# Kernel optimization log

Measured on AMD Instinct MI355X. Metric: run time of the kernel, lower is better.

Reference implementation:

```python
import jax, jax.numpy as jnp
import numpy as np

ROUTING_ITERS = 3

def squash(t, axis=-1):
    norm = jnp.linalg.norm(t, axis=axis, keepdims=True)
    scale = norm ** 2 / (1 + norm ** 2)
    return scale * t / (norm + 1e-08)

def setup_inputs() -> dict:
    key = jax.random.key(0)
    k1, k2 = jax.random.split(key)
    B, R, C, Din, Dout = 64, 4608, 32, 16, 16
    x = jax.random.normal(k1, (B, R, Din), dtype=jnp.float32)
    route_weights = jax.random.normal(k2, (R, C, Din, Dout), dtype=jnp.float32)
    return {"x": x, "route_weights": route_weights}

def reference(x, route_weights):
    # x: [B, R, Din], route_weights: [R, C, Din, Dout]
    B, R, _ = x.shape
    C = route_weights.shape[1]
    # u_hat: [B, R, C, Dout]  (prediction vectors)
    u_hat = jnp.einsum('bri,rcio->brco', x, route_weights)
    b_ij = jnp.zeros((B, R, C, 1), dtype=u_hat.dtype)
    v_j = None
    for _ in range(ROUTING_ITERS):
        c_ij = jax.nn.softmax(b_ij, axis=2)                    # coupling coeffs over capsules
        s_j = jnp.sum(c_ij * u_hat, axis=1, keepdims=True)     # [B, 1, C, Dout]
        v_j = squash(s_j, axis=-1)                             # [B, 1, C, Dout]
        b_ij = b_ij + jnp.sum(u_hat * v_j, axis=-1, keepdims=True)
    return v_j[:, 0]                                           # [B, C, Dout]
```

## Files before the change

kernel.cpp:

```cpp
#include <hip/hip_runtime.h>
#include <math.h>


#define B_    64
#define R_    4608
#define C_    32
#define RB    18
#define NBLK  (R_ / RB)
#define SELEM 32768

typedef _Float16 half8  __attribute__((ext_vector_type(8)));
typedef _Float16 half2v __attribute__((ext_vector_type(2)));
typedef float    f32x16 __attribute__((ext_vector_type(16)));

__device__ __forceinline__ void gload_lds16(const void* g, void* l) {
    __builtin_amdgcn_global_load_lds(
        (const __attribute__((address_space(1))) void*)g,
        (__attribute__((address_space(3))) void*)l, 16, 0, 0);
}

__global__ __launch_bounds__(256)
void caps_prep(const float* __restrict__ x, _Float16* __restrict__ xa)
{
    const int idx = blockIdx.x * 256 + threadIdx.x;
    const int r = idx >> 6, b = idx & 63;
    const float4* xs = (const float4*)(x + ((size_t)b * R_ + r) * 16);
    const float4 A = xs[0], Bv = xs[1], Cv = xs[2], Dv = xs[3];
    half8 lo, hi;
    lo[0]=(_Float16)A.x;  lo[1]=(_Float16)A.y;  lo[2]=(_Float16)A.z;  lo[3]=(_Float16)A.w;
    lo[4]=(_Float16)Bv.x; lo[5]=(_Float16)Bv.y; lo[6]=(_Float16)Bv.z; lo[7]=(_Float16)Bv.w;
    hi[0]=(_Float16)Cv.x; hi[1]=(_Float16)Cv.y; hi[2]=(_Float16)Cv.z; hi[3]=(_Float16)Cv.w;
    hi[4]=(_Float16)Dv.x; hi[5]=(_Float16)Dv.y; hi[6]=(_Float16)Dv.z; hi[7]=(_Float16)Dv.w;
    half8* dst = (half8*)(xa + ((size_t)idx << 4));
    dst[0] = lo; dst[1] = hi;
}

__global__ __launch_bounds__(512)
void caps_wprep(const float* __restrict__ W, _Float16* __restrict__ wp)
{
    __shared__ float wl[2][8192];
    const int tid = threadIdx.x;
    const int rb  = blockIdx.x * 2;

#pragma unroll
    for (int rr = 0; rr < 2; ++rr)
#pragma unroll
        for (int k = 0; k < 4; ++k)
            gload_lds16((const char*)W + (size_t)(rb + rr) * 32768 + k * 8192 + tid * 16,
                        (char*)wl[rr] + k * 8192 + tid * 16);
    asm volatile("s_waitcnt vmcnt(0)" ::: "memory");
    __syncthreads();

    const int lane = tid & 63;
    const int h    = lane >> 5;
    const int l31  = lane & 31;
    const int o    = l31 & 15;

#pragma unroll
    for (int rr = 0; rr < 2; ++rr) {
#pragma unroll
        for (int ci = 0; ci < 2; ++ci) {
            const int nt = ci * 8 + (tid >> 6);
            const int c  = 2 * nt + (l31 >> 4);
            half8 f;
#pragma unroll
            for (int e = 0; e < 8; ++e)
                f[e] = (_Float16)wl[rr][c * 256 + (8 * h + e) * 16 + o];
            *(half8*)(wp + (((size_t)(rb + rr) * 16 + nt) * 64 + lane) * 8) = f;
        }
    }
}

template<bool FIRST>
__global__ __launch_bounds__(512, 4)
void caps_mfma(const _Float16* __restrict__ xa, const _Float16* __restrict__ wp,
               const float* __restrict__ vsumT, float* __restrict__ sdst)
{
    __shared__ _Float16 xalds[RB * 512];
    __shared__ float t_lds[32][33];
    __shared__ float c_lds[32][33];

    const int tid  = threadIdx.x;
    const int lane = tid & 63;
    const int wv   = tid >> 6;
    const int h    = lane >> 5;
    const int l31  = lane & 31;
    const int bh   = blockIdx.y;
    const int r0   = blockIdx.x * RB;
    const int bg   = bh * 32 + l31;

    {
        const int slx = (lane << 4) ^ (((lane >> 3) & 7) << 4);
        for (int t = wv; t < RB; t += 8) {
            const char* src = (const char*)xa + (size_t)(r0 + t) * 2048 + bh * 1024 + slx;
            gload_lds16(src, (char*)xalds + t * 1024);
        }
    }

    f32x16 sacc0, sacc1, zf;
#pragma unroll
    for (int k = 0; k < 16; ++k) { sacc0[k] = 0.f; sacc1[k] = 0.f; zf[k] = 0.f; }

    half2v vh[2][8];
    if (!FIRST) {
#pragma unroll
        for (int j = 0; j < 2; ++j)
#pragma unroll
            for (int e = 0; e < 16; ++e) {
                const int g = (2 * wv + j) * 32 + (e & 3) + 8 * (e >> 2) + 4 * h;
                vh[j][e >> 1][e & 1] = (_Float16)vsumT[(size_t)g * 64 + bg];
            }
    }

    asm volatile("s_waitcnt vmcnt(0)" ::: "memory");
    __syncthreads();

    const int avoff = ((l31 << 5) + (h << 4)) ^ (((l31 >> 2) & 7) << 4);

    const size_t wstride = 16 * 64 * 8;
    const _Float16* wpb = wp + (((size_t)r0 * 16 + 2 * wv) * 64 + lane) * 8;
    half8 bc0 = *(const half8*)wpb;
    half8 bc1 = *(const half8*)(wpb + 512);

#pragma unroll 1
    for (int t = 0; t < RB; ++t) {
        const half8 av = *(const half8*)((const char*)xalds + t * 1024 + avoff);

        f32x16 u0, u1;
        if (FIRST) {
            sacc0 = __builtin_amdgcn_mfma_f32_32x32x16_f16(bc0, av, sacc0, 0, 0, 0);
            sacc1 = __builtin_amdgcn_mfma_f32_32x32x16_f16(bc1, av, sacc1, 0, 0, 0);
        } else {
            u0 = __builtin_amdgcn_mfma_f32_32x32x16_f16(bc0, av, zf, 0, 0, 0);
            u1 = __builtin_amdgcn_mfma_f32_32x32x16_f16(bc1, av, zf, 0, 0, 0);
        }

        const int tn = (t < RB - 1) ? (t + 1) : t;
        const _Float16* wpn = wp + ((size_t)(r0 + tn)) * wstride + ((size_t)(2 * wv) * 64 + lane) * 8;
        bc0 = *(const half8*)wpn;
        bc1 = *(const half8*)(wpn + 512);

        if (FIRST) continue;

        float tc[2][2];
#pragma unroll
        for (int j = 0; j < 2; ++j) {
            const f32x16& u = j ? u1 : u0;
            float s0 = 0.f, s1 = 0.f;
#pragma unroll
            for (int e2 = 0; e2 < 4; ++e2) {
                s0 += u[2 * e2]     * (float)vh[j][e2][0];
                s0 += u[2 * e2 + 1] * (float)vh[j][e2][1];
                s1 += u[8 + 2 * e2]     * (float)vh[j][4 + e2][0];
                s1 += u[8 + 2 * e2 + 1] * (float)vh[j][4 + e2][1];
            }
            s0 += __shfl_xor(s0, 32);
            s1 += __shfl_xor(s1, 32);
            tc[j][0] = s0; tc[j][1] = s1;
        }
        if (h == 0) {
            t_lds[4 * wv    ][l31] = tc[0][0];
            t_lds[4 * wv + 1][l31] = tc[0][1];
            t_lds[4 * wv + 2][l31] = tc[1][0];
            t_lds[4 * wv + 3][l31] = tc[1][1];
        }
        __syncthreads();

        {
            const int a_ = lane & 15;
            const int b2 = tid >> 4;
            const float tA = t_lds[2 * a_][b2];
            const float tB = t_lds[2 * a_ + 1][b2];
            float m = fmaxf(tA, tB);
            m = fmaxf(m, __shfl_xor(m, 1));
            m = fmaxf(m, __shfl_xor(m, 2));
            m = fmaxf(m, __shfl_xor(m, 4));
            m = fmaxf(m, __shfl_xor(m, 8));
            const float eA = __expf(tA - m);
            const float eB = __expf(tB - m);
            float zs = eA + eB;
            zs += __shfl_xor(zs, 1);
            zs += __shfl_xor(zs, 2);
            zs += __shfl_xor(zs, 4);
            zs += __shfl_xor(zs, 8);
            const float inv = 1.0f / zs;
            c_lds[2 * a_][b2]     = eA * inv;
            c_lds[2 * a_ + 1][b2] = eB * inv;
        }
        __syncthreads();

#pragma unroll
        for (int j = 0; j < 2; ++j) {
            const f32x16& u = j ? u1 : u0;
            f32x16& sa = j ? sacc1 : sacc0;
            const float c0v = c_lds[4 * wv + 2 * j    ][l31];
            const float c1v = c_lds[4 * wv + 2 * j + 1][l31];
#pragma unroll
            for (int e = 0; e < 8; ++e)  sa[e]     += c0v * u[e];
#pragma unroll
            for (int e = 8; e < 16; ++e) sa[e]     += c1v * u[e];
        }
    }

    const float scale = FIRST ? 0.03125f : 1.0f;
    float* sp = sdst + ((size_t)blockIdx.x << 15);
#pragma unroll
    for (int j = 0; j < 2; ++j) {
        const f32x16& sa = j ? sacc1 : sacc0;
#pragma unroll
        for (int e = 0; e < 16; ++e) {
            const int g = (2 * wv + j) * 32 + (e & 3) + 8 * (e >> 2) + 4 * h;
            sp[(size_t)g * 64 + bg] = sa[e] * scale;
        }
    }
}

__global__ __launch_bounds__(256)
void caps_reduce1(const float* __restrict__ sp, float* __restrict__ s2)
{
    const int e  = blockIdx.x * 256 + threadIdx.x;
    const int pg = blockIdx.y;
    const float* p0 = sp + (size_t)pg * 32 * SELEM + e;
    float a = 0.0f;
#pragma unroll 8
    for (int p = 0; p < 32; ++p) a += p0[(size_t)p * SELEM];
    s2[pg * SELEM + e] = a;
}

__global__ __launch_bounds__(64)
void caps_reduce2T(const float* __restrict__ src, float* __restrict__ vsumT,
                   float* __restrict__ out, int mode)
{
    const int c = blockIdx.x;
    const int b = threadIdx.x;
    float a[16];
#pragma unroll
    for (int o = 0; o < 16; ++o) a[o] = 0.0f;
    for (int p = 0; p < 8; ++p)
#pragma unroll
        for (int o = 0; o < 16; ++o)
            a[o] += src[(size_t)p * SELEM + c * 1024 + o * 64 + b];
    float sq = 0.0f;
#pragma unroll
    for (int o = 0; o < 16; ++o) sq += a[o] * a[o];
    const float n  = sqrtf(sq);
    const float sc = sq / (1.0f + sq) / (n + 1e-8f);
    if (mode == 2) {
#pragma unroll
        for (int o = 0; o < 16; ++o)
            out[(size_t)b * 512 + c * 16 + o] = a[o] * sc;
    } else if (mode == 0) {
#pragma unroll
        for (int o = 0; o < 16; ++o)
            vsumT[c * 1024 + o * 64 + b] = a[o] * sc;
    } else {
#pragma unroll
        for (int o = 0; o < 16; ++o)
            vsumT[c * 1024 + o * 64 + b] += a[o] * sc;
    }
}

__global__ __launch_bounds__(256)
void caps_reduce2(const float* __restrict__ src, int P,
                  float* __restrict__ vsum, float* __restrict__ out, int mode)
{
    const int e = blockIdx.x * 256 + threadIdx.x;
    float a = 0.0f;
    for (int p = 0; p < P; ++p) a += src[(size_t)p * SELEM + e];
    float sq = a * a;
#pragma unroll
    for (int off = 8; off >= 1; off >>= 1) sq += __shfl_xor(sq, off);
    const float n = sqrtf(sq);
    const float v = a * (sq / (1.0f + sq) / (n + 1e-8f));
    if (mode == 0)      vsum[e] = v;
    else if (mode == 1) vsum[e] += v;
    else                out[e] = v;
}

template<bool FIRST>
__global__ __launch_bounds__(1024, 4)
void caps_pass_f32(const float* __restrict__ x, const float* __restrict__ W,
                   const float* __restrict__ vsumg, float* __restrict__ sdst)
{
    __shared__ float wlds[2][8192];
    const int tid = threadIdx.x, lane = tid & 63;
    const int c = tid & 31, dh = (tid >> 5) & 1, w = tid >> 6;
    const int r0 = blockIdx.x * RB, b0 = w << 2;
    const int key = (c & 7) << 4;
    const int cb  = (c << 10) + (dh << 5);

    float sacc[4][8];
#pragma unroll
    for (int q = 0; q < 4; ++q)
#pragma unroll
        for (int k = 0; k < 8; ++k) sacc[q][k] = 0.0f;

    float vreg[4][8];
    if (!FIRST) {
#pragma unroll
        for (int q = 0; q < 4; ++q) {
            const float4* vp = (const float4*)(vsumg + ((((b0+q) << 5) + c) << 4) + (dh << 3));
            float4 a = vp[0], bq = vp[1];
            vreg[q][0]=a.x; vreg[q][1]=a.y; vreg[q][2]=a.z; vreg[q][3]=a.w;
            vreg[q][4]=bq.x; vreg[q][5]=bq.y; vreg[q][6]=bq.z; vreg[q][7]=bq.w;
        }
    }

    const int Dloc0 = (w << 11);
    const int lx0 = (lane << 4) ^ ((((w << 1))     & 7) << 4);
    const int lx1 = (lane << 4) ^ ((((w << 1) | 1) & 7) << 4);
    const int wu = __builtin_amdgcn_readfirstlane(w);
    const float* xw = x + (size_t)((wu << 2) * R_ + r0) * 16;

#define STAGE(buf, r)                                                              \
    do {                                                                           \
        const char* wr_ = (const char*)W + ((size_t)(r) << 15);                    \
        gload_lds16(wr_ + Dloc0        + lx0, (char*)wlds[buf] + Dloc0);           \
        gload_lds16(wr_ + Dloc0 + 1024 + lx1, (char*)wlds[buf] + Dloc0 + 1024);    \
    } while (0)

    STAGE(0, r0);
#pragma unroll 1
    for (int t = 0; t < RB; ++t) {
        const int cur = t & 1;
        if (t + 1 < RB) { STAGE(cur ^ 1, r0 + t + 1); asm volatile("s_waitcnt vmcnt(2)" ::: "memory"); }
        else            { asm volatile("s_waitcnt vmcnt(0)" ::: "memory"); }
        __builtin_amdgcn_s_barrier();
        __builtin_amdgcn_sched_barrier(0);

        const char* lb = (const char*)wlds[cur];
        float u[4][8];
#pragma unroll
        for (int q = 0; q < 4; ++q)
#pragma unroll
            for (int k = 0; k < 8; ++k) u[q][k] = 0.0f;

#pragma unroll
        for (int i = 0; i < 16; ++i) {
            const int A = (cb + (i << 6)) ^ key;
            float4 w0 = *(const float4*)(lb + A);
            float4 w1 = *(const float4*)(lb + (A ^ 16));
            float wv[8] = {w0.x, w0.y, w0.z, w0.w, w1.x, w1.y, w1.z, w1.w};
#pragma unroll
            for (int q = 0; q < 4; ++q) {
                const float xv = xw[(size_t)q * (R_ * 16) + t * 16 + i];
#pragma unroll
                for (int k = 0; k < 8; ++k) u[q][k] = fmaf(xv, wv[k], u[q][k]);
            }
        }

#pragma unroll
        for (int q = 0; q < 4; ++q) {
            float cij;
            if (FIRST) cij = 0.03125f;
            else {
                float th = 0.0f;
#pragma unroll
                for (int k = 0; k < 8; ++k) th = fmaf(u[q][k], vreg[q][k], th);
                th += __shfl_xor(th, 32);
                float m = th;
#pragma unroll
                for (int off = 16; off >= 1; off >>= 1) m = fmaxf(m, __shfl_xor(m, off));
                const float e = __expf(th - m);
                float ssum = e;
#pragma unroll
                for (int off = 16; off >= 1; off >>= 1) ssum += __shfl_xor(ssum, off);
                cij = e / ssum;
            }
#pragma unroll
            for (int k = 0; k < 8; ++k) sacc[q][k] = fmaf(cij, u[q][k], sacc[q][k]);
        }
        __builtin_amdgcn_s_barrier();
    }
#undef STAGE

#pragma unroll
    for (int q = 0; q < 4; ++q) {
        float* sp = sdst + ((((b0+q) << 5) + c) << 4) + (dh << 3);
#pragma unroll
        for (int k = 0; k < 8; ++k) atomicAdd(sp + k, sacc[q][k]);
    }
}

extern "C" void kernel_launch(void* const* d_in, const int* in_sizes, int n_in,
                              void* d_out, int out_size, void* d_ws, size_t ws_size,
                              hipStream_t stream)
{
    const float* x = (const float*)d_in[0];
    const float* W = (const float*)d_in[1];
    float* out = (float*)d_out;

    const size_t WPB = (size_t)R_ * 16 * 64 * 8 * sizeof(_Float16);
    const size_t XAB = (size_t)R_ * 64 * 16 * sizeof(_Float16);
    const size_t SPB = (size_t)NBLK * SELEM * sizeof(float);
    const size_t S2B = (size_t)8 * SELEM * sizeof(float);
    const size_t VSB = (size_t)SELEM * sizeof(float);
    char* wsc = (char*)d_ws;
    const dim3 pgrid(NBLK, 2);

    if (ws_size >= WPB + XAB + SPB + S2B + VSB) {
        _Float16* wp  = (_Float16*)wsc;
        _Float16* xa  = (_Float16*)(wsc + WPB);
        float* s_part = (float*)(wsc + WPB + XAB);
        float* s2     = (float*)(wsc + WPB + XAB + SPB);
        float* vsumT  = (float*)(wsc + WPB + XAB + SPB + S2B);

        caps_prep<<<1152, 256, 0, stream>>>(x, xa);
        caps_wprep<<<R_ / 2, 512, 0, stream>>>(W, wp);

        caps_mfma<true ><<<pgrid, 512, 0, stream>>>(xa, wp, nullptr, s_part);
        caps_reduce1<<<dim3(128, 8), 256, 0, stream>>>(s_part, s2);
        caps_reduce2T<<<32, 64, 0, stream>>>(s2, vsumT, nullptr, 0);

        caps_mfma<false><<<pgrid, 512, 0, stream>>>(xa, wp, vsumT, s_part);
        caps_reduce1<<<dim3(128, 8), 256, 0, stream>>>(s_part, s2);
        caps_reduce2T<<<32, 64, 0, stream>>>(s2, vsumT, nullptr, 1);

        caps_mfma<false><<<pgrid, 512, 0, stream>>>(xa, wp, vsumT, s_part);
        caps_reduce1<<<dim3(128, 8), 256, 0, stream>>>(s_part, s2);
        caps_reduce2T<<<32, 64, 0, stream>>>(s2, vsumT, out, 2);
    } else {
        float* s    = (float*)wsc;
        float* vsum = s + SELEM;

        hipMemsetAsync(s, 0, VSB, stream);
        caps_pass_f32<true><<<NBLK, 1024, 0, stream>>>(x, W, nullptr, s);
        caps_reduce2<<<128, 256, 0, stream>>>(s, 1, vsum, nullptr, 0);

        hipMemsetAsync(s, 0, VSB, stream);
        caps_pass_f32<false><<<NBLK, 1024, 0, stream>>>(x, W, vsum, s);
        caps_reduce2<<<128, 256, 0, stream>>>(s, 1, vsum, nullptr, 1);

        hipMemsetAsync(s, 0, VSB, stream);
        caps_pass_f32<false><<<NBLK, 1024, 0, stream>>>(x, W, vsum, s);
        caps_reduce2<<<128, 256, 0, stream>>>(s, 1, nullptr, out, 2);
    }
}
```

Before: 156.7 us.

## Use 1024-thread routing blocks with one capsule-pair tile per wave, fuse prep kernels

The routing kernel moves from 512 threads with two MFMA tiles per wave to 1024 threads with one tile per wave. It also doubles the route block size to 36, which halves the partial sums and reduce1's per-group loop. The x and W fp16 conversion kernels are merged into one launch. The aim is lower per-wave register pressure, more latency hiding, and fewer launches and partial-sum traffic, at the cost of half as many blocks and heavier block-wide syncs. The __launch_bounds__(1024,4) hint may also constrain registers.

```diff
diff --git a/kernel.cpp b/kernel.cpp
--- a/kernel.cpp
+++ b/kernel.cpp
@@ -5,7 +5,7 @@
 #define B_    64
 #define R_    4608
 #define C_    32
-#define RB    18
+#define RB    36
 #define NBLK  (R_ / RB)
 #define SELEM 32768
 
@@ -19,28 +19,28 @@
         (__attribute__((address_space(3))) void*)l, 16, 0, 0);
 }
 
-__global__ __launch_bounds__(256)
-void caps_prep(const float* __restrict__ x, _Float16* __restrict__ xa)
-{
-    const int idx = blockIdx.x * 256 + threadIdx.x;
-    const int r = idx >> 6, b = idx & 63;
-    const float4* xs = (const float4*)(x + ((size_t)b * R_ + r) * 16);
-    const float4 A = xs[0], Bv = xs[1], Cv = xs[2], Dv = xs[3];
-    half8 lo, hi;
-    lo[0]=(_Float16)A.x;  lo[1]=(_Float16)A.y;  lo[2]=(_Float16)A.z;  lo[3]=(_Float16)A.w;
-    lo[4]=(_Float16)Bv.x; lo[5]=(_Float16)Bv.y; lo[6]=(_Float16)Bv.z; lo[7]=(_Float16)Bv.w;
-    hi[0]=(_Float16)Cv.x; hi[1]=(_Float16)Cv.y; hi[2]=(_Float16)Cv.z; hi[3]=(_Float16)Cv.w;
-    hi[4]=(_Float16)Dv.x; hi[5]=(_Float16)Dv.y; hi[6]=(_Float16)Dv.z; hi[7]=(_Float16)Dv.w;
-    half8* dst = (half8*)(xa + ((size_t)idx << 4));
-    dst[0] = lo; dst[1] = hi;
-}
-
 __global__ __launch_bounds__(512)
-void caps_wprep(const float* __restrict__ W, _Float16* __restrict__ wp)
-{
+void caps_conv(const float* __restrict__ W, const float* __restrict__ x,
+               _Float16* __restrict__ wp, _Float16* __restrict__ xa)
+{
+    const int tid = threadIdx.x;
+    if (blockIdx.x >= 2304) {
+        const int idx = (blockIdx.x - 2304) * 512 + tid;
+        const int r = idx >> 6, b = idx & 63;
+        const float4* xs = (const float4*)(x + ((size_t)b * R_ + r) * 16);
+        const float4 A = xs[0], Bv = xs[1], Cv = xs[2], Dv = xs[3];
+        half8 lo, hi;
+        lo[0]=(_Float16)A.x;  lo[1]=(_Float16)A.y;  lo[2]=(_Float16)A.z;  lo[3]=(_Float16)A.w;
+        lo[4]=(_Float16)Bv.x; lo[5]=(_Float16)Bv.y; lo[6]=(_Float16)Bv.z; lo[7]=(_Float16)Bv.w;
+        hi[0]=(_Float16)Cv.x; hi[1]=(_Float16)Cv.y; hi[2]=(_Float16)Cv.z; hi[3]=(_Float16)Cv.w;
+        hi[4]=(_Float16)Dv.x; hi[5]=(_Float16)Dv.y; hi[6]=(_Float16)Dv.z; hi[7]=(_Float16)Dv.w;
+        half8* dst = (half8*)(xa + ((size_t)idx << 4));
+        dst[0] = lo; dst[1] = hi;
+        return;
+    }
+
     __shared__ float wl[2][8192];
-    const int tid = threadIdx.x;
-    const int rb  = blockIdx.x * 2;
+    const int rb = blockIdx.x * 2;
 
 #pragma unroll
     for (int rr = 0; rr < 2; ++rr)
@@ -72,7 +72,7 @@
 }
 
 template<bool FIRST>
-__global__ __launch_bounds__(512, 4)
+__global__ __launch_bounds__(1024, 4)
 void caps_mfma(const _Float16* __restrict__ xa, const _Float16* __restrict__ wp,
                const float* __restrict__ vsumT, float* __restrict__ sdst)
 {
@@ -91,25 +91,23 @@
 
     {
         const int slx = (lane << 4) ^ (((lane >> 3) & 7) << 4);
-        for (int t = wv; t < RB; t += 8) {
+        for (int t = wv; t < RB; t += 16) {
             const char* src = (const char*)xa + (size_t)(r0 + t) * 2048 + bh * 1024 + slx;
             gload_lds16(src, (char*)xalds + t * 1024);
         }
     }
 
-    f32x16 sacc0, sacc1, zf;
-#pragma unroll
-    for (int k = 0; k < 16; ++k) { sacc0[k] = 0.f; sacc1[k] = 0.f; zf[k] = 0.f; }
-
-    half2v vh[2][8];
+    f32x16 sacc, zf;
+#pragma unroll
+    for (int k = 0; k < 16; ++k) { sacc[k] = 0.f; zf[k] = 0.f; }
+
+    half2v vh[8];
     if (!FIRST) {
 #pragma unroll
-        for (int j = 0; j < 2; ++j)
-#pragma unroll
-            for (int e = 0; e < 16; ++e) {
-                const int g = (2 * wv + j) * 32 + (e & 3) + 8 * (e >> 2) + 4 * h;
-                vh[j][e >> 1][e & 1] = (_Float16)vsumT[(size_t)g * 64 + bg];
-            }
+        for (int e = 0; e < 16; ++e) {
+            const int g = wv * 32 + (e & 3) + 8 * (e >> 2) + 4 * h;
+            vh[e >> 1][e & 1] = (_Float16)vsumT[(size_t)g * 64 + bg];
+        }
     }
 
     asm volatile("s_waitcnt vmcnt(0)" ::: "memory");
@@ -118,55 +116,45 @@
     const int avoff = ((l31 << 5) + (h << 4)) ^ (((l31 >> 2) & 7) << 4);
 
     const size_t wstride = 16 * 64 * 8;
-    const _Float16* wpb = wp + (((size_t)r0 * 16 + 2 * wv) * 64 + lane) * 8;
-    half8 bc0 = *(const half8*)wpb;
-    half8 bc1 = *(const half8*)(wpb + 512);
+    const _Float16* wpb = wp + (((size_t)r0 * 16 + wv) * 64 + lane) * 8;
+    half8 bc = *(const half8*)wpb;
 
 #pragma unroll 1
     for (int t = 0; t < RB; ++t) {
         const half8 av = *(const half8*)((const char*)xalds + t * 1024 + avoff);
 
-        f32x16 u0, u1;
+        f32x16 u;
         if (FIRST) {
-            sacc0 = __builtin_amdgcn_mfma_f32_32x32x16_f16(bc0, av, sacc0, 0, 0, 0);
-            sacc1 = __builtin_amdgcn_mfma_f32_32x32x16_f16(bc1, av, sacc1, 0, 0, 0);
+            sacc = __builtin_amdgcn_mfma_f32_32x32x16_f16(bc, av, sacc, 0, 0, 0);
         } else {
-            u0 = __builtin_amdgcn_mfma_f32_32x32x16_f16(bc0, av, zf, 0, 0, 0);
-            u1 = __builtin_amdgcn_mfma_f32_32x32x16_f16(bc1, av, zf, 0, 0, 0);
+            u = __builtin_amdgcn_mfma_f32_32x32x16_f16(bc, av, zf, 0, 0, 0);
         }
 
         const int tn = (t < RB - 1) ? (t + 1) : t;
-        const _Float16* wpn = wp + ((size_t)(r0 + tn)) * wstride + ((size_t)(2 * wv) * 64 + lane) * 8;
-        bc0 = *(const half8*)wpn;
-        bc1 = *(const half8*)(wpn + 512);
+        bc = *(const half8*)(wp + ((size_t)(r0 + tn)) * wstride
+                                + ((size_t)wv * 64 + lane) * 8);
 
         if (FIRST) continue;
 
-        float tc[2][2];
-#pragma unroll
-        for (int j = 0; j < 2; ++j) {
-            const f32x16& u = j ? u1 : u0;
+        {
             float s0 = 0.f, s1 = 0.f;
 #pragma unroll
             for (int e2 = 0; e2 < 4; ++e2) {
-                s0 += u[2 * e2]     * (float)vh[j][e2][0];
-                s0 += u[2 * e2 + 1] * (float)vh[j][e2][1];
-                s1 += u[8 + 2 * e2]     * (float)vh[j][4 + e2][0];
-                s1 += u[8 + 2 * e2 + 1] * (float)vh[j][4 + e2][1];
+                s0 += u[2 * e2]         * (float)vh[e2][0];
+                s0 += u[2 * e2 + 1]     * (float)vh[e2][1];
+                s1 += u[8 + 2 * e2]     * (float)vh[4 + e2][0];
+                s1 += u[8 + 2 * e2 + 1] * (float)vh[4 + e2][1];
             }
             s0 += __shfl_xor(s0, 32);
             s1 += __shfl_xor(s1, 32);
-            tc[j][0] = s0; tc[j][1] = s1;
-        }
-        if (h == 0) {
-            t_lds[4 * wv    ][l31] = tc[0][0];
-            t_lds[4 * wv + 1][l31] = tc[0][1];
-            t_lds[4 * wv + 2][l31] = tc[1][0];
-            t_lds[4 * wv + 3][l31] = tc[1][1];
+            if (h == 0) {
+                t_lds[2 * wv    ][l31] = s0;
+                t_lds[2 * wv + 1][l31] = s1;
+            }
         }
         __syncthreads();
 
-        {
+        if (tid < 512) {
             const int a_ = lane & 15;
             const int b2 = tid >> 4;
             const float tA = t_lds[2 * a_][b2];
@@ -189,29 +177,22 @@
         }
         __syncthreads();
 
-#pragma unroll
-        for (int j = 0; j < 2; ++j) {
-            const f32x16& u = j ? u1 : u0;
-            f32x16& sa = j ? sacc1 : sacc0;
-            const float c0v = c_lds[4 * wv + 2 * j    ][l31];
-            const float c1v = c_lds[4 * wv + 2 * j + 1][l31];
-#pragma unroll
-            for (int e = 0; e < 8; ++e)  sa[e]     += c0v * u[e];
-#pragma unroll
-            for (int e = 8; e < 16; ++e) sa[e]     += c1v * u[e];
+        {
+            const float c0v = c_lds[2 * wv    ][l31];
+            const float c1v = c_lds[2 * wv + 1][l31];
+#pragma unroll
+            for (int e = 0; e < 8; ++e)  sacc[e] += c0v * u[e];
+#pragma unroll
+            for (int e = 8; e < 16; ++e) sacc[e] += c1v * u[e];
         }
     }
 
     const float scale = FIRST ? 0.03125f : 1.0f;
     float* sp = sdst + ((size_t)blockIdx.x << 15);
 #pragma unroll
-    for (int j = 0; j < 2; ++j) {
-        const f32x16& sa = j ? sacc1 : sacc0;
-#pragma unroll
-        for (int e = 0; e < 16; ++e) {
-            const int g = (2 * wv + j) * 32 + (e & 3) + 8 * (e >> 2) + 4 * h;
-            sp[(size_t)g * 64 + bg] = sa[e] * scale;
-        }
+    for (int e = 0; e < 16; ++e) {
+        const int g = wv * 32 + (e & 3) + 8 * (e >> 2) + 4 * h;
+        sp[(size_t)g * 64 + bg] = sacc[e] * scale;
     }
 }
 
@@ -220,10 +201,10 @@
 {
     const int e  = blockIdx.x * 256 + threadIdx.x;
     const int pg = blockIdx.y;
-    const float* p0 = sp + (size_t)pg * 32 * SELEM + e;
+    const float* p0 = sp + (size_t)pg * 16 * SELEM + e;
     float a = 0.0f;
 #pragma unroll 8
-    for (int p = 0; p < 32; ++p) a += p0[(size_t)p * SELEM];
+    for (int p = 0; p < 16; ++p) a += p0[(size_t)p * SELEM];
     s2[pg * SELEM + e] = a;
 }
 
@@ -405,18 +386,17 @@
         float* s2     = (float*)(wsc + WPB + XAB + SPB);
         float* vsumT  = (float*)(wsc + WPB + XAB + SPB + S2B);
 
-        caps_prep<<<1152, 256, 0, stream>>>(x, xa);
-        caps_wprep<<<R_ / 2, 512, 0, stream>>>(W, wp);
-
-        caps_mfma<true ><<<pgrid, 512, 0, stream>>>(xa, wp, nullptr, s_part);
+        caps_conv<<<2304 + 576, 512, 0, stream>>>(W, x, wp, xa);
+
+        caps_mfma<true ><<<pgrid, 1024, 0, stream>>>(xa, wp, nullptr, s_part);
         caps_reduce1<<<dim3(128, 8), 256, 0, stream>>>(s_part, s2);
         caps_reduce2T<<<32, 64, 0, stream>>>(s2, vsumT, nullptr, 0);
 
-        caps_mfma<false><<<pgrid, 512, 0, stream>>>(xa, wp, vsumT, s_part);
+        caps_mfma<false><<<pgrid, 1024, 0, stream>>>(xa, wp, vsumT, s_part);
         caps_reduce1<<<dim3(128, 8), 256, 0, stream>>>(s_part, s2);
         caps_reduce2T<<<32, 64, 0, stream>>>(s2, vsumT, nullptr, 1);
 
-        caps_mfma<false><<<pgrid, 512, 0, stream>>>(xa, wp, vsumT, s_part);
+        caps_mfma<false><<<pgrid, 1024, 0, stream>>>(xa, wp, vsumT, s_part);
         caps_reduce1<<<dim3(128, 8), 256, 0, stream>>>(s_part, s2);
         caps_reduce2T<<<32, 64, 0, stream>>>(s2, vsumT, out, 2);
     } else {
```

Measured after the change: 159.4 us. Within noise of the previous version (+1.7%).
